# Kernel optimization log

Measured on AMD Instinct MI355X. Metric: run time of the kernel, lower is better.

The kernel has to match this reference:

```python
import jax, jax.numpy as jnp
import numpy as np

D_MODEL = 1024
D_FF = 4096
N_EXPERTS = 8
TOP_K = 2

def setup_inputs() -> dict:
    key = jax.random.key(0)
    ks = jax.random.split(key, 6)
    s = lambda fan_in: 1.0 / np.sqrt(fan_in)
    x = jax.random.normal(ks[0], (4, 2048, D_MODEL), dtype=jnp.float32)
    Wg = jax.random.normal(ks[1], (D_MODEL, N_EXPERTS), dtype=jnp.float32) * s(D_MODEL)
    W1 = jax.random.normal(ks[2], (N_EXPERTS, D_MODEL, D_FF), dtype=jnp.float32) * s(D_MODEL)
    b1 = jax.random.normal(ks[3], (N_EXPERTS, D_FF), dtype=jnp.float32) * 0.01
    W2 = jax.random.normal(ks[4], (N_EXPERTS, D_FF, D_MODEL), dtype=jnp.float32) * s(D_FF)
    b2 = jax.random.normal(ks[5], (N_EXPERTS, D_MODEL), dtype=jnp.float32) * 0.01
    return {"x": x, "Wg": Wg, "W1": W1, "b1": b1, "W2": W2, "b2": b2}

def reference(x, Wg, W1, b1, W2, b2):
    B, L, D = x.shape
    xf = x.reshape(B * L, D)               # (N, D)
    N = xf.shape[0]
    E = Wg.shape[1]
    # gating
    logits = xf @ Wg                        # (N, E)
    probs = jax.nn.softmax(logits, axis=-1)
    topv, topi = jax.lax.top_k(probs, TOP_K)          # (N, K)
    w = topv / (topv.sum(axis=-1, keepdims=True) + 1e-9)
    rows = jnp.arange(N)[:, None]
    combine = jnp.zeros((N, E), xf.dtype).at[rows, topi].set(w)    # (N, E) combine weights
    dispatch = jnp.zeros((N, E), xf.dtype).at[rows, topi].set(1.0)
    aux_loss = (dispatch.mean(axis=0) * probs.mean(axis=0)).sum() * E
    # experts: dense per-expert FFN, masked-combined (zero weight => zero contribution),
    # mathematically identical to the torch masked gather/scatter loop.
    out = jnp.zeros_like(xf)
    for e in range(E):  # fixed small loop over experts
        h = jax.nn.gelu(xf @ W1[e] + b1[e], approximate=False)   # (N, d_ff)
        out = out + combine[:, e:e + 1] * (h @ W2[e] + b2[e])
    return out.reshape(B, L, D), aux_loss
```

## Files before the change

kernel.cpp:

```cpp
#include <hip/hip_runtime.h>
#include <math.h>

#define D_MODEL 1024
#define D_FF    4096
#define NEXP    8
#define NTOK    8192
#define NASSIGN (NTOK*2)
#define NGBLK   (NTOK/4)

using short8 = __attribute__((ext_vector_type(8))) short;
using short4v = __attribute__((ext_vector_type(4))) short;
using f32x4  = __attribute__((ext_vector_type(4))) float;

__device__ __forceinline__ short f2bf(float f) {
  unsigned u = __float_as_uint(f);
  unsigned r = (u + 0x7fffu + ((u >> 16) & 1u)) >> 16;
  return (short)r;
}

__device__ __forceinline__ void gload_lds16(const void* g, void* l) {
  __builtin_amdgcn_global_load_lds((const __attribute__((address_space(1))) void*)g,
                                   (__attribute__((address_space(3))) void*)l, 16, 0, 0);
}

__device__ __forceinline__ float gelu_f(float x) {
  float z = 0.70710678118f * x;
  float a = fabsf(z);
  float t = 1.0f / (1.0f + 0.3275911f * a);
  float p = t * (0.254829592f + t * (-0.284496736f + t * (1.421413741f +
            t * (-1.453152027f + t * 1.061405429f))));
  float er = 1.0f - p * __expf(-a * a);
  er = copysignf(er, z);
  return 0.5f * x * (1.0f + er);
}

__global__ void zero_kernel(int* ctrl) {
  int i = threadIdx.x;
  if (i < 24) ctrl[i] = 0;
}

__global__ __launch_bounds__(256) void transpose_conv(const float* __restrict__ in, short* __restrict__ out,
                                                      int R, int C) {
  __shared__ float t[64][65];
  int e = blockIdx.z;
  size_t base = (size_t)e * R * C;
  int r0 = blockIdx.y * 64, c0 = blockIdx.x * 64;
  int lr = threadIdx.x >> 6, lc = threadIdx.x & 63;
#pragma unroll
  for (int j = 0; j < 16; ++j) {
    int rr = lr + j * 4;
    t[rr][lc] = in[base + (size_t)(r0 + rr) * C + c0 + lc];
  }
  __syncthreads();
#pragma unroll
  for (int j = 0; j < 16; ++j) {
    int oc = lr + j * 4;
    out[base + (size_t)(c0 + oc) * R + r0 + lc] = f2bf(t[lc][oc]);
  }
}

__global__ __launch_bounds__(256) void gating_kernel(const float* __restrict__ x, const float* __restrict__ Wg,
                                                     int* __restrict__ assign_e, float* __restrict__ assign_w,
                                                     int* __restrict__ cnt_part, float* __restrict__ psum_part,
                                                     ushort4* __restrict__ xb4) {
  __shared__ float l_ps[NEXP];
  __shared__ int   l_cnt[NEXP];
  int tid = threadIdx.x, wv = tid >> 6, lane = tid & 63;
  if (tid < NEXP) { l_ps[tid] = 0.f; l_cnt[tid] = 0; }
  __syncthreads();

  int t = blockIdx.x * 4 + wv;
  const float4* xr = (const float4*)(x + (size_t)t * D_MODEL);
  float acc[NEXP];
#pragma unroll
  for (int e = 0; e < NEXP; ++e) acc[e] = 0.f;
#pragma unroll
  for (int i = 0; i < 4; ++i) {
    int c4 = lane + 64 * i;
    float4 v = xr[c4];
    ushort4 o;
    o.x = (unsigned short)f2bf(v.x); o.y = (unsigned short)f2bf(v.y);
    o.z = (unsigned short)f2bf(v.z); o.w = (unsigned short)f2bf(v.w);
    xb4[(size_t)t * 256 + c4] = o;
    const float* wr = Wg + c4 * 4 * NEXP;
#pragma unroll
    for (int j = 0; j < 4; ++j) {
      float xv = (&v.x)[j];
#pragma unroll
      for (int e = 0; e < NEXP; ++e) acc[e] += xv * wr[j * NEXP + e];
    }
  }
#pragma unroll
  for (int off = 32; off; off >>= 1)
#pragma unroll
    for (int e = 0; e < NEXP; ++e) acc[e] += __shfl_down(acc[e], off);

  if (lane == 0) {
    float m = acc[0];
#pragma unroll
    for (int e = 1; e < NEXP; ++e) m = fmaxf(m, acc[e]);
    float p[NEXP], s = 0.f;
#pragma unroll
    for (int e = 0; e < NEXP; ++e) { p[e] = expf(acc[e] - m); s += p[e]; }
    float inv = 1.f / s;
#pragma unroll
    for (int e = 0; e < NEXP; ++e) p[e] *= inv;
    int i0 = 0; float v0 = p[0];
#pragma unroll
    for (int e = 1; e < NEXP; ++e) if (p[e] > v0) { v0 = p[e]; i0 = e; }
    int i1 = -1; float v1 = -1.f;
#pragma unroll
    for (int e = 0; e < NEXP; ++e) if (e != i0 && p[e] > v1) { v1 = p[e]; i1 = e; }
    float denom = 1.f / (v0 + v1 + 1e-9f);
    assign_e[2 * t] = i0;     assign_w[2 * t] = v0 * denom;
    assign_e[2 * t + 1] = i1; assign_w[2 * t + 1] = v1 * denom;
    atomicAdd(&l_cnt[i0], 1);
    atomicAdd(&l_cnt[i1], 1);
#pragma unroll
    for (int e = 0; e < NEXP; ++e) atomicAdd(&l_ps[e], p[e]);
  }
  __syncthreads();
  if (tid < NEXP) {
    psum_part[blockIdx.x * NEXP + tid] = l_ps[tid];
    cnt_part[blockIdx.x * NEXP + tid] = l_cnt[tid];
  }
}

__global__ __launch_bounds__(256) void scan_kernel(const int* __restrict__ cnt_part, const float* __restrict__ psum_part,
                                                   int* __restrict__ cnt, int* __restrict__ offs,
                                                   float* __restrict__ aux_out) {
  __shared__ float sp[256];
  __shared__ int   sc[256];
  int tid = threadIdx.x;
  int e = tid & 7, c = tid >> 3;
  float fs = 0.f; int is = 0;
  for (int b = c; b < NGBLK; b += 32) {
    fs += psum_part[b * NEXP + e];
    is += cnt_part[b * NEXP + e];
  }
  sp[tid] = fs; sc[tid] = is;
  __syncthreads();
  if (tid < NEXP) {
    float f = 0.f; int n = 0;
    for (int c2 = 0; c2 < 32; ++c2) { f += sp[c2 * 8 + tid]; n += sc[c2 * 8 + tid]; }
    cnt[tid] = n; sp[tid] = f;
  }
  __syncthreads();
  if (tid == 0) {
    int o = 0; float aux = 0.f;
    for (int e2 = 0; e2 < NEXP; ++e2) {
      offs[e2] = o; o += cnt[e2];
      aux += (float)cnt[e2] * sp[e2];
    }
    aux_out[0] = aux * (float)NEXP / ((float)NTOK * (float)NTOK);
  }
}

__global__ __launch_bounds__(256) void scatter_kernel(const int* __restrict__ assign_e,
                                                      const int* __restrict__ offs, int* __restrict__ cursor,
                                                      int* __restrict__ slot_tok, int* __restrict__ slot_of) {
  __shared__ int lhist[NEXP], lbase[NEXP];
  int tid = threadIdx.x;
  int a = blockIdx.x * 256 + tid;
  if (tid < NEXP) lhist[tid] = 0;
  __syncthreads();
  int e = assign_e[a];
  int lp = atomicAdd(&lhist[e], 1);
  __syncthreads();
  if (tid < NEXP) lbase[tid] = atomicAdd(&cursor[tid], lhist[tid]);
  __syncthreads();
  int s = offs[e] + lbase[e] + lp;
  slot_tok[s] = a >> 1;
  slot_of[a] = s;
}

template<int KD, int ND, int RT, int EPI>
__global__ __launch_bounds__(512, 2) void gemm8p(
    const short* __restrict__ Asrc, const short* __restrict__ Bsrc,
    const float* __restrict__ bias, const int* __restrict__ slot_tok,
    const int* __restrict__ cnt, const int* __restrict__ offs,
    void* __restrict__ OutP)
{
  constexpr int NT = KD / 64;
  constexpr int NP = ND / 256;
  extern __shared__ char ldsb[];

  int bid = blockIdx.x;
  int x = bid & 7, j = bid >> 3;
  int k = j / RT, rt = j % RT;
  int ft = k % NP;
  int e = (x + k) & 7;
  int cn = cnt[e];
  if (rt * 256 >= cn) return;
  int off = offs[e];
  int tid = threadIdx.x, l = tid & 63, w = tid >> 6;
  int wm = w >> 2, wn = w & 3;
  int l15 = l & 15, kh = l >> 4;

  int srw = tid >> 3;
  int swz = ((tid & 7) ^ (srw & 7)) * 8;
  const short* ar[4];
  const short* br[4];
#pragma unroll
  for (int s = 0; s < 4; ++s) {
    int gr = rt * 256 + s * 64 + srw;
    int ic = gr < cn ? gr : cn - 1;
    if (EPI == 0) ar[s] = Asrc + (size_t)slot_tok[off + ic] * KD + swz;
    else          ar[s] = Asrc + (size_t)(off + ic) * KD + swz;
    br[s] = Bsrc + (size_t)e * ND * KD + (size_t)(ft * 256 + s * 64 + srw) * KD + swz;
  }

#define STAGE(P, TAU) do {                                                        \
    int _b = (TAU) & 1;                                                           \
    const short* _p0 = ((P) >= 2 ? ar : br)[(P) & 1];                             \
    const short* _p1 = ((P) >= 2 ? ar : br)[((P) & 1) + 2];                       \
    char* _d = ldsb + _b * 65536 + ((P) >= 2 ? 0 : 32768);                        \
    gload_lds16(_p0 + (size_t)(TAU) * 64, _d + ((P) & 1) * 8192 + tid * 16);      \
    gload_lds16(_p1 + (size_t)(TAU) * 64, _d + (((P) & 1) + 2) * 8192 + tid * 16);\
  } while (0)

  STAGE(0, 0); STAGE(1, 0); STAGE(2, 0); STAGE(3, 0);
  STAGE(0, 1);
  asm volatile("s_waitcnt vmcnt(2)" ::: "memory");
  asm volatile("s_barrier" ::: "memory");

  int cx0 = ((0 * 4 + kh) ^ (l15 & 7)) << 4;
  int cx1 = ((1 * 4 + kh) ^ (l15 & 7)) << 4;
  int arow = (wm * 128 + l15) << 7;
  int brow = (wn * 64 + l15) << 7;
  f32x4 acc[8][4] = {};
  short8 bqA[4], bqB[4], afA[4], afB[4];

  for (int t = 0; t < NT; ++t) {
    const char* Ab = ldsb + (t & 1) * 65536;
    const char* Bb = Ab + 32768;
#pragma unroll
    for (int n = 0; n < 4; ++n) bqA[n] = *(const short8*)(Bb + brow + (n << 11) + cx0);
#pragma unroll
    for (int m = 0; m < 4; ++m) afA[m] = *(const short8*)(Ab + arow + ((m * 16) << 7) + cx0);
    if (t + 1 < NT) STAGE(1, t + 1);
#pragma unroll
    for (int m = 0; m < 4; ++m) afB[m] = *(const short8*)(Ab + arow + ((64 + m * 16) << 7) + cx0);
    asm volatile("s_barrier" ::: "memory");
    __builtin_amdgcn_s_setprio(1);
#pragma unroll
    for (int m = 0; m < 4; ++m)
#pragma unroll
      for (int n = 0; n < 4; ++n)
        acc[m][n] = __builtin_amdgcn_mfma_f32_16x16x32_bf16(bqA[n], afA[m], acc[m][n], 0, 0, 0);
    __builtin_amdgcn_s_setprio(0);
    asm volatile("s_barrier" ::: "memory");
    if (t + 1 < NT) STAGE(2, t + 1);
#pragma unroll
    for (int m = 0; m < 4; ++m) afA[m] = *(const short8*)(Ab + arow + ((m * 16) << 7) + cx1);
#pragma unroll
    for (int n = 0; n < 4; ++n) bqB[n] = *(const short8*)(Bb + brow + (n << 11) + cx1);
    asm volatile("s_barrier" ::: "memory");
    __builtin_amdgcn_s_setprio(1);
#pragma unroll
    for (int m = 0; m < 4; ++m)
#pragma unroll
      for (int n = 0; n < 4; ++n)
        acc[4 + m][n] = __builtin_amdgcn_mfma_f32_16x16x32_bf16(bqA[n], afB[m], acc[4 + m][n], 0, 0, 0);
    __builtin_amdgcn_s_setprio(0);
    asm volatile("s_barrier" ::: "memory");
    if (t + 1 < NT) STAGE(3, t + 1);
#pragma unroll
    for (int m = 0; m < 4; ++m) afB[m] = *(const short8*)(Ab + arow + ((64 + m * 16) << 7) + cx1);
    asm volatile("s_barrier" ::: "memory");
    __builtin_amdgcn_s_setprio(1);
#pragma unroll
    for (int m = 0; m < 4; ++m)
#pragma unroll
      for (int n = 0; n < 4; ++n)
        acc[m][n] = __builtin_amdgcn_mfma_f32_16x16x32_bf16(bqB[n], afA[m], acc[m][n], 0, 0, 0);
    __builtin_amdgcn_s_setprio(0);
    asm volatile("s_barrier" ::: "memory");
    if (t + 2 < NT) STAGE(0, t + 2);
    asm volatile("s_barrier" ::: "memory");
    __builtin_amdgcn_s_setprio(1);
#pragma unroll
    for (int m = 0; m < 4; ++m)
#pragma unroll
      for (int n = 0; n < 4; ++n)
        acc[4 + m][n] = __builtin_amdgcn_mfma_f32_16x16x32_bf16(bqB[n], afB[m], acc[4 + m][n], 0, 0, 0);
    __builtin_amdgcn_s_setprio(0);
    if (t < NT - 2)       { asm volatile("s_waitcnt vmcnt(2)" ::: "memory"); }
    else if (t == NT - 2) { asm volatile("s_waitcnt vmcnt(0)" ::: "memory"); }
    asm volatile("s_barrier" ::: "memory");
  }
#undef STAGE

  int ftb = ft * 256;
  f32x4 b4[4];
#pragma unroll
  for (int n = 0; n < 4; ++n) b4[n] = *(const f32x4*)&bias[e * ND + ftb + wn * 64 + n * 16 + kh * 4];

  if (EPI == 1) {
    float* Y = (float*)OutP;
#pragma unroll
    for (int mi = 0; mi < 8; ++mi) {
      int tok = rt * 256 + wm * 128 + mi * 16 + l15;
      if (tok < cn) {
#pragma unroll
        for (int n = 0; n < 4; ++n) {
          f32x4 o;
#pragma unroll
          for (int jj = 0; jj < 4; ++jj) o[jj] = acc[mi][n][jj] + b4[n][jj];
          *(f32x4*)&Y[(size_t)(off + tok) * ND + ftb + wn * 64 + n * 16 + kh * 4] = o;
        }
      }
    }
  } else {
    short* H = (short*)OutP;
    char* slab = ldsb + w * 2048;
#pragma unroll
    for (int mi = 0; mi < 8; ++mi) {
#pragma unroll
      for (int n = 0; n < 4; ++n) {
        short4v h;
#pragma unroll
        for (int jj = 0; jj < 4; ++jj) h[jj] = f2bf(gelu_f(acc[mi][n][jj] + b4[n][jj]));
        int chunk = n * 2 + (kh >> 1);
        *(short4v*)(slab + l15 * 128 + ((chunk ^ (l15 & 7)) << 4) + ((kh & 1) << 3)) = h;
      }
      int tr = l >> 2;
      int tok = rt * 256 + wm * 128 + mi * 16 + tr;
      if (tok < cn) {
#pragma unroll
        for (int cc = 0; cc < 2; ++cc) {
          int c2 = (l & 3) * 2 + cc;
          short8 v = *(const short8*)(slab + tr * 128 + ((c2 ^ (tr & 7)) << 4));
          *(short8*)&H[(size_t)(off + tok) * ND + ftb + wn * 64 + c2 * 8] = v;
        }
      }
      asm volatile("s_waitcnt lgkmcnt(0)" ::: "memory");
    }
  }
}

__global__ __launch_bounds__(256) void combine_kernel(const float* __restrict__ y, const int* __restrict__ slot_of,
                                                      const float* __restrict__ assign_w, float* __restrict__ out) {
  int t = blockIdx.x;
  int d4 = threadIdx.x;
  int s0 = slot_of[2 * t], s1 = slot_of[2 * t + 1];
  float w0 = assign_w[2 * t], w1 = assign_w[2 * t + 1];
  float4 a = ((const float4*)(y + (size_t)s0 * D_MODEL))[d4];
  float4 b = ((const float4*)(y + (size_t)s1 * D_MODEL))[d4];
  float4 o;
  o.x = w0 * a.x + w1 * b.x;
  o.y = w0 * a.y + w1 * b.y;
  o.z = w0 * a.z + w1 * b.z;
  o.w = w0 * a.w + w1 * b.w;
  ((float4*)(out + (size_t)t * D_MODEL))[d4] = o;
}

extern "C" void kernel_launch(void* const* d_in, const int* in_sizes, int n_in,
                              void* d_out, int out_size, void* d_ws, size_t ws_size,
                              hipStream_t stream) {
  const float* x  = (const float*)d_in[0];
  const float* Wg = (const float*)d_in[1];
  const float* W1 = (const float*)d_in[2];
  const float* b1 = (const float*)d_in[3];
  const float* W2 = (const float*)d_in[4];
  const float* b2 = (const float*)d_in[5];
  float* out = (float*)d_out;
  char* ws = (char*)d_ws;

  short* xb       = (short*)(ws);
  short* w1t      = (short*)(ws + 16777216);
  float* y        = (float*)(ws + 16777216);
  short* w2t      = (short*)(ws + 83886080);
  short* H        = (short*)(ws + 150994944);
  int*   slot_tok = (int*)  (ws + 285212672);
  int*   assign_e = (int*)  (ws + 285278208);
  float* assign_w = (float*)(ws + 285343744);
  int*   slot_of  = (int*)  (ws + 285409280);
  int*   cnt_part = (int*)  (ws + 285474816);
  float* psum_part= (float*)(ws + 285540352);
  int*   ctrl     = (int*)  (ws + 285605888);
  int* cnt = ctrl; int* cursor = ctrl + 8; int* offs = ctrl + 16;

  hipFuncSetAttribute(reinterpret_cast<const void*>(&gemm8p<D_MODEL, D_FF, 12, 0>),
                      hipFuncAttributeMaxDynamicSharedMemorySize, 131072);
  hipFuncSetAttribute(reinterpret_cast<const void*>(&gemm8p<D_FF, D_MODEL, 12, 1>),
                      hipFuncAttributeMaxDynamicSharedMemorySize, 131072);

  zero_kernel<<<1, 64, 0, stream>>>(ctrl);
  transpose_conv<<<dim3(64, 16, NEXP), 256, 0, stream>>>(W1, w1t, D_MODEL, D_FF);
  transpose_conv<<<dim3(16, 64, NEXP), 256, 0, stream>>>(W2, w2t, D_FF, D_MODEL);
  gating_kernel<<<NGBLK, 256, 0, stream>>>(x, Wg, assign_e, assign_w, cnt_part, psum_part,
                                           (ushort4*)xb);
  scan_kernel<<<1, 256, 0, stream>>>(cnt_part, psum_part, cnt, offs, out + (out_size - 1));
  scatter_kernel<<<NASSIGN / 256, 256, 0, stream>>>(assign_e, offs, cursor, slot_tok, slot_of);
  gemm8p<D_MODEL, D_FF, 12, 0><<<8 * 16 * 12, 512, 131072, stream>>>(
      xb, w1t, b1, slot_tok, cnt, offs, H);
  gemm8p<D_FF, D_MODEL, 12, 1><<<8 * 4 * 12, 512, 131072, stream>>>(
      H, w2t, b2, slot_tok, cnt, offs, y);
  combine_kernel<<<NTOK, 256, 0, stream>>>(y, slot_of, assign_w, out);
}
```

Measured before the change: 555.6 us.

## Store second GEMM output as bf16, vectorize transpose stores, reorder tile mapping

The second expert GEMM now writes its output in bf16 through the same LDS-staged epilogue as the first GEMM, and the combine kernel reads bf16 and widens it to fp32. This halves the traffic for the intermediate y buffer, at the cost of extra rounding before the weighted combine. The weight transpose-convert kernel now writes 16-byte vectors of bf16 instead of scalar shorts. The second GEMM's block-index mapping switches to row-tile-outer ordering, which changes L2 reuse of the weight panels.

```diff
diff --git a/kernel.cpp b/kernel.cpp
--- a/kernel.cpp
+++ b/kernel.cpp
@@ -16,6 +16,9 @@
   unsigned u = __float_as_uint(f);
   unsigned r = (u + 0x7fffu + ((u >> 16) & 1u)) >> 16;
   return (short)r;
+}
+__device__ __forceinline__ float bf2f(unsigned short u) {
+  return __uint_as_float(((unsigned)u) << 16);
 }
 
 __device__ __forceinline__ void gload_lds16(const void* g, void* l) {
@@ -52,10 +55,15 @@
     t[rr][lc] = in[base + (size_t)(r0 + rr) * C + c0 + lc];
   }
   __syncthreads();
-#pragma unroll
-  for (int j = 0; j < 16; ++j) {
-    int oc = lr + j * 4;
-    out[base + (size_t)(c0 + oc) * R + r0 + lc] = f2bf(t[lc][oc]);
+  int tid = threadIdx.x;
+#pragma unroll
+  for (int p = 0; p < 2; ++p) {
+    int oc = p * 32 + (tid >> 3);
+    int rseg = (tid & 7) * 8;
+    short8 v;
+#pragma unroll
+    for (int q = 0; q < 8; ++q) v[q] = f2bf(t[rseg + q][oc]);
+    *(short8*)&out[base + (size_t)(c0 + oc) * R + r0 + rseg] = v;
   }
 }
 
@@ -174,20 +182,23 @@
   slot_of[a] = s;
 }
 
-template<int KD, int ND, int RT, int EPI>
+template<int KD, int ND, int RT, int EPI, bool RTOUT>
 __global__ __launch_bounds__(512, 2) void gemm8p(
     const short* __restrict__ Asrc, const short* __restrict__ Bsrc,
     const float* __restrict__ bias, const int* __restrict__ slot_tok,
     const int* __restrict__ cnt, const int* __restrict__ offs,
-    void* __restrict__ OutP)
+    short* __restrict__ OutP)
 {
   constexpr int NT = KD / 64;
   constexpr int NP = ND / 256;
+  constexpr int NPAN = NEXP * NP / 8;
   extern __shared__ char ldsb[];
 
   int bid = blockIdx.x;
   int x = bid & 7, j = bid >> 3;
-  int k = j / RT, rt = j % RT;
+  int k, rt;
+  if (RTOUT) { rt = j / NPAN; k = j - rt * NPAN; }
+  else       { k = j / RT;    rt = j - k * RT; }
   int ft = k % NP;
   int e = (x + k) & 7;
   int cn = cnt[e];
@@ -296,62 +307,49 @@
 #pragma unroll
   for (int n = 0; n < 4; ++n) b4[n] = *(const f32x4*)&bias[e * ND + ftb + wn * 64 + n * 16 + kh * 4];
 
-  if (EPI == 1) {
-    float* Y = (float*)OutP;
-#pragma unroll
-    for (int mi = 0; mi < 8; ++mi) {
-      int tok = rt * 256 + wm * 128 + mi * 16 + l15;
-      if (tok < cn) {
-#pragma unroll
-        for (int n = 0; n < 4; ++n) {
-          f32x4 o;
-#pragma unroll
-          for (int jj = 0; jj < 4; ++jj) o[jj] = acc[mi][n][jj] + b4[n][jj];
-          *(f32x4*)&Y[(size_t)(off + tok) * ND + ftb + wn * 64 + n * 16 + kh * 4] = o;
-        }
+  char* slab = ldsb + w * 2048;
+#pragma unroll
+  for (int mi = 0; mi < 8; ++mi) {
+#pragma unroll
+    for (int n = 0; n < 4; ++n) {
+      short4v h;
+#pragma unroll
+      for (int jj = 0; jj < 4; ++jj) {
+        float v = acc[mi][n][jj] + b4[n][jj];
+        if (EPI == 0) v = gelu_f(v);
+        h[jj] = f2bf(v);
+      }
+      int chunk = n * 2 + (kh >> 1);
+      *(short4v*)(slab + l15 * 128 + ((chunk ^ (l15 & 7)) << 4) + ((kh & 1) << 3)) = h;
+    }
+    int tr = l >> 2;
+    int tok = rt * 256 + wm * 128 + mi * 16 + tr;
+    if (tok < cn) {
+#pragma unroll
+      for (int cc = 0; cc < 2; ++cc) {
+        int c2 = (l & 3) * 2 + cc;
+        short8 v = *(const short8*)(slab + tr * 128 + ((c2 ^ (tr & 7)) << 4));
+        *(short8*)&OutP[(size_t)(off + tok) * ND + ftb + wn * 64 + c2 * 8] = v;
       }
     }
-  } else {
-    short* H = (short*)OutP;
-    char* slab = ldsb + w * 2048;
-#pragma unroll
-    for (int mi = 0; mi < 8; ++mi) {
-#pragma unroll
-      for (int n = 0; n < 4; ++n) {
-        short4v h;
-#pragma unroll
-        for (int jj = 0; jj < 4; ++jj) h[jj] = f2bf(gelu_f(acc[mi][n][jj] + b4[n][jj]));
-        int chunk = n * 2 + (kh >> 1);
-        *(short4v*)(slab + l15 * 128 + ((chunk ^ (l15 & 7)) << 4) + ((kh & 1) << 3)) = h;
-      }
-      int tr = l >> 2;
-      int tok = rt * 256 + wm * 128 + mi * 16 + tr;
-      if (tok < cn) {
-#pragma unroll
-        for (int cc = 0; cc < 2; ++cc) {
-          int c2 = (l & 3) * 2 + cc;
-          short8 v = *(const short8*)(slab + tr * 128 + ((c2 ^ (tr & 7)) << 4));
-          *(short8*)&H[(size_t)(off + tok) * ND + ftb + wn * 64 + c2 * 8] = v;
-        }
-      }
-      asm volatile("s_waitcnt lgkmcnt(0)" ::: "memory");
-    }
-  }
-}
-
-__global__ __launch_bounds__(256) void combine_kernel(const float* __restrict__ y, const int* __restrict__ slot_of,
+    asm volatile("s_waitcnt lgkmcnt(0)" ::: "memory");
+  }
+}
+
+__global__ __launch_bounds__(256) void combine_kernel(const unsigned short* __restrict__ y,
+                                                      const int* __restrict__ slot_of,
                                                       const float* __restrict__ assign_w, float* __restrict__ out) {
   int t = blockIdx.x;
   int d4 = threadIdx.x;
   int s0 = slot_of[2 * t], s1 = slot_of[2 * t + 1];
   float w0 = assign_w[2 * t], w1 = assign_w[2 * t + 1];
-  float4 a = ((const float4*)(y + (size_t)s0 * D_MODEL))[d4];
-  float4 b = ((const float4*)(y + (size_t)s1 * D_MODEL))[d4];
+  ushort4 a = ((const ushort4*)(y + (size_t)s0 * D_MODEL))[d4];
+  ushort4 b = ((const ushort4*)(y + (size_t)s1 * D_MODEL))[d4];
   float4 o;
-  o.x = w0 * a.x + w1 * b.x;
-  o.y = w0 * a.y + w1 * b.y;
-  o.z = w0 * a.z + w1 * b.z;
-  o.w = w0 * a.w + w1 * b.w;
+  o.x = w0 * bf2f(a.x) + w1 * bf2f(b.x);
+  o.y = w0 * bf2f(a.y) + w1 * bf2f(b.y);
+  o.z = w0 * bf2f(a.z) + w1 * bf2f(b.z);
+  o.w = w0 * bf2f(a.w) + w1 * bf2f(b.w);
   ((float4*)(out + (size_t)t * D_MODEL))[d4] = o;
 }
 
@@ -369,7 +367,7 @@
 
   short* xb       = (short*)(ws);
   short* w1t      = (short*)(ws + 16777216);
-  float* y        = (float*)(ws + 16777216);
+  short* y        = (short*)(ws + 16777216);
   short* w2t      = (short*)(ws + 83886080);
   short* H        = (short*)(ws + 150994944);
   int*   slot_tok = (int*)  (ws + 285212672);
@@ -381,9 +379,9 @@
   int*   ctrl     = (int*)  (ws + 285605888);
   int* cnt = ctrl; int* cursor = ctrl + 8; int* offs = ctrl + 16;
 
-  hipFuncSetAttribute(reinterpret_cast<const void*>(&gemm8p<D_MODEL, D_FF, 12, 0>),
+  hipFuncSetAttribute(reinterpret_cast<const void*>(&gemm8p<D_MODEL, D_FF, 12, 0, false>),
                       hipFuncAttributeMaxDynamicSharedMemorySize, 131072);
-  hipFuncSetAttribute(reinterpret_cast<const void*>(&gemm8p<D_FF, D_MODEL, 12, 1>),
+  hipFuncSetAttribute(reinterpret_cast<const void*>(&gemm8p<D_FF, D_MODEL, 12, 1, true>),
                       hipFuncAttributeMaxDynamicSharedMemorySize, 131072);
 
   zero_kernel<<<1, 64, 0, stream>>>(ctrl);
@@ -393,9 +391,9 @@
                                            (ushort4*)xb);
   scan_kernel<<<1, 256, 0, stream>>>(cnt_part, psum_part, cnt, offs, out + (out_size - 1));
   scatter_kernel<<<NASSIGN / 256, 256, 0, stream>>>(assign_e, offs, cursor, slot_tok, slot_of);
-  gemm8p<D_MODEL, D_FF, 12, 0><<<8 * 16 * 12, 512, 131072, stream>>>(
+  gemm8p<D_MODEL, D_FF, 12, 0, false><<<8 * 16 * 12, 512, 131072, stream>>>(
       xb, w1t, b1, slot_tok, cnt, offs, H);
-  gemm8p<D_FF, D_MODEL, 12, 1><<<8 * 4 * 12, 512, 131072, stream>>>(
+  gemm8p<D_FF, D_MODEL, 12, 1, true><<<8 * 4 * 12, 512, 131072, stream>>>(
       H, w2t, b2, slot_tok, cnt, offs, y);
-  combine_kernel<<<NTOK, 256, 0, stream>>>(y, slot_of, assign_w, out);
-}
+  combine_kernel<<<NTOK, 256, 0, stream>>>((const unsigned short*)y, slot_of, assign_w, out);
+}
```

New measurement: 558.6 us. No clear change (+0.5%).
